# Kernel optimization log

Measured on AMD Instinct MI355X. Metric: run time of the kernel, lower is better.

Reference implementation:

```python
import jax, jax.numpy as jnp
import numpy as np

B = 8
C_IN = 3
DIV = 7
N0 = 20 * 4 ** DIV      # 327680 pixels at division 7
N1 = N0 // 4            # 81920 pixels at division 6
N2 = N1 // 4            # 20480 pixels at division 5
K_CONV = 10             # SpherePHD conv kernel size (triangle + 9 neighbors)
K_ADJ = 4               # pooling neighborhood (pixel + 3 edge-adjacent)


def setup_inputs() -> dict:
    key = jax.random.key(0)
    ks = jax.random.split(key, 15)
    x = jax.random.normal(ks[0], (B, C_IN, N0), dtype=jnp.float32)
    conv_t0 = jax.random.randint(ks[1], (N0, K_CONV), 0, N0, dtype=jnp.int32)
    conv_t1 = jax.random.randint(ks[2], (N1, K_CONV), 0, N1, dtype=jnp.int32)
    conv_t2 = jax.random.randint(ks[3], (N2, K_CONV), 0, N2, dtype=jnp.int32)
    adj0 = jax.random.randint(ks[4], (N0, K_ADJ), 0, N0, dtype=jnp.int32)
    adj1 = jax.random.randint(ks[5], (N1, K_ADJ), 0, N1, dtype=jnp.int32)
    pool0 = jax.random.randint(ks[6], (N1,), 0, N0, dtype=jnp.int32)
    pool1 = jax.random.randint(ks[7], (N2,), 0, N1, dtype=jnp.int32)
    w1 = jax.random.normal(ks[8], (16, C_IN, K_CONV), dtype=jnp.float32) * 0.1
    b1 = jax.random.normal(ks[9], (16,), dtype=jnp.float32) * 0.1
    w2 = jax.random.normal(ks[10], (32, 16, K_CONV), dtype=jnp.float32) * 0.1
    b2 = jax.random.normal(ks[11], (32,), dtype=jnp.float32) * 0.1
    w3 = jax.random.normal(ks[12], (10, 32, K_CONV), dtype=jnp.float32) * 0.1
    b3 = jax.random.normal(ks[13], (10,), dtype=jnp.float32) * 0.1
    return {"x": x, "conv_t0": conv_t0, "conv_t1": conv_t1, "conv_t2": conv_t2,
            "adj0": adj0, "adj1": adj1, "pool0": pool0, "pool1": pool1,
            "w1": w1, "b1": b1, "w2": w2, "b2": b2, "w3": w3, "b3": b3}


def phd_conv2d(x, table, w, b):
    # x: [B, Cin, N]; table: [N, K] neighbor indices; w: [Cout, Cin, K]
    g = x[:, :, table]                               # gather -> [B, Cin, N, K]
    return jnp.einsum('bcnk,ock->bon', g, w) + b[None, :, None]


def phd_maxpool(x, adj, pool):
    # max over adjacency neighborhood, then 4:1 downsample via pooling table
    m = jnp.max(x[:, :, adj], axis=-1)               # [B, C, N_fine]
    return m[:, :, pool]                             # [B, C, N_coarse]


def reference(x, conv_t0, conv_t1, conv_t2, adj0, adj1, pool0, pool1,
              w1, b1, w2, b2, w3, b3):
    h = phd_conv2d(x, conv_t0, w1, b1)               # [B, 16, N0]
    h = phd_maxpool(h, adj0, pool0)                  # [B, 16, N1]
    h = phd_conv2d(h, conv_t1, w2, b2)               # [B, 32, N1]
    h = phd_maxpool(h, adj1, pool1)                  # [B, 32, N2]
    h = phd_conv2d(h, conv_t2, w3, b3)               # [B, 10, N2]
    return jnp.mean(h, axis=-1)                      # PHD_avgpool -> [B, 10]
```

## Files before the change

### kernel.cpp

```cpp
#include <hip/hip_runtime.h>

#define NB 8
#define CIN 3
#define N0 327680
#define N1 81920
#define N2 20480
#define KC 10
#define KA 4

typedef __attribute__((ext_vector_type(8))) short bf16x8;
typedef __attribute__((ext_vector_type(4))) float f32x4;
typedef int4  __attribute__((aligned(4))) int4_u;

__device__ __forceinline__ unsigned f2bf(float f) {
  unsigned u = __float_as_uint(f);
  return (u + 0x7FFFu + ((u >> 16) & 1u)) >> 16;
}

union bfrag { bf16x8 v; unsigned u[4]; };

__global__ __launch_bounds__(256) void kpre(
    const float* __restrict__ x, uint4* __restrict__ xT64,
    const int* __restrict__ conv_t0, const int* __restrict__ conv_t1,
    const int* __restrict__ conv_t2,
    const int* __restrict__ adj0, const int* __restrict__ adj1,
    const int* __restrict__ pool0, const int* __restrict__ pool1,
    int* __restrict__ fidxM, int* __restrict__ fidxP, float* __restrict__ A12,
    const float* __restrict__ w1, const float* __restrict__ w2,
    const float* __restrict__ w3, const float* __restrict__ b3,
    unsigned short* __restrict__ wB1, unsigned short* __restrict__ wB,
    float* __restrict__ w3t, float* __restrict__ out) {
  int blk = blockIdx.x;
  if (blk < 1280) {
    int n = blk * 256 + threadIdx.x;
    unsigned d[12];
#pragma unroll
    for (int bp = 0; bp < 4; ++bp) {
      const float* pe = x + (size_t)(2 * bp) * CIN * N0 + n;
      const float* po = pe + (size_t)CIN * N0;
      float e0 = pe[0], e1 = pe[N0], e2 = pe[2 * N0];
      float o0 = po[0], o1 = po[N0], o2 = po[2 * N0];
      d[bp * 3 + 0] = f2bf(e0) | (f2bf(e1) << 16);
      d[bp * 3 + 1] = f2bf(e2) | (f2bf(o0) << 16);
      d[bp * 3 + 2] = f2bf(o1) | (f2bf(o2) << 16);
    }
    uint4* dst = xT64 + (size_t)n * 4;
    dst[0] = make_uint4(d[0], d[1], d[2], d[3]);
    dst[1] = make_uint4(d[4], d[5], d[6], d[7]);
    dst[2] = make_uint4(d[8], d[9], d[10], d[11]);
    dst[3] = make_uint4(0, 0, 0, 0);
  } else if (blk < 2560) {
    int t = (blk - 1280) * 256 + threadIdx.x;
    int j = t >> 2, p = t & 3;
    int pj = pool0[j];
    int pos = adj0[pj * KA + p];
    const int2* s0 = (const int2*)(conv_t0 + (size_t)pos * 10);
    int2 q0 = s0[0], q1 = s0[1], q2 = s0[2], q3 = s0[3], q4 = s0[4];
    int4_u* dM = (int4_u*)(fidxM + (size_t)t * 12);
    dM[0] = make_int4(q0.x * 64, q0.y * 64, q4.x * 64, q4.y * 64);
    dM[1] = make_int4(q1.x * 64, q1.y * 64, q2.x * 64, q2.y * 64);
    dM[2] = make_int4(q3.x * 64, q3.y * 64, 0, 0);
    if (j < N2) {
      int qj = pool1[j];
      int qos = adj1[qj * KA + p];
      const int2* s1 = (const int2*)(conv_t1 + (size_t)qos * 10);
      int2 r0 = s1[0], r1 = s1[1], r2 = s1[2], r3 = s1[3], r4 = s1[4];
      int4_u* dP = (int4_u*)(fidxP + (size_t)t * 12);
      dP[0] = make_int4(r0.x * 32, r1.x * 32, r2.x * 32, r3.x * 32);
      dP[1] = make_int4(r4.x * 32, 0,          r0.y * 32, r1.y * 32);
      dP[2] = make_int4(r2.y * 32, r3.y * 32, r4.y * 32, 0);
    }
  } else if (blk < 3360) {
    int t = (blk - 2560) * 256 + threadIdx.x;
    int n = conv_t2[t];
    int k = t % 10;
    atomicAdd(&A12[n * 12 + k], 1.0f);
  } else {
    int t = (blk - 3360) * 256 + threadIdx.x;
    if (t < 1024) {
      int ch = t >> 9, rest = t & 511, l = rest >> 3, e = rest & 7;
      int k = ch * 32 + ((l >> 4) * 8) + e;
      int tap = k >> 2, cc = k & 3;
      float v = (tap < KC && cc < CIN) ? w1[((l & 15) * CIN + cc) * KC + tap] : 0.f;
      wB1[t] = (unsigned short)f2bf(v);
    }
    if (t < 5120) {
      int e = t & 7, l = (t >> 3) & 63, nt = (t >> 9) & 1, q = t >> 10;
      int kc = q * 32 + ((l >> 4) * 8) + e;
      int tap = kc >> 4, c = kc & 15;
      int o = nt * 16 + (l & 15);
      wB[t] = (unsigned short)f2bf(w2[(o * 16 + c) * KC + tap]);
    }
    if (t < 3200) { int o = t % 10, r = t / 10, c = r & 31, k = r >> 5;
                    w3t[t] = w3[(o * 32 + c) * KC + k]; }
    if (t < 80)   out[t] = b3[t % 10];
  }
}

#define TR0(s) ((s) == 0 ? Ra.x : (s) == 1 ? Ra.w : (s) == 2 ? Rb.z : Rc.y)
#define TR1(s) ((s) == 0 ? Ra.y : (s) == 1 ? Rb.x : (s) == 2 ? Rb.w : Rc.z)
#define TR2(s) ((s) == 0 ? Ra.z : (s) == 1 ? Rb.y : (s) == 2 ? Rc.x : Rc.w)

__global__ __launch_bounds__(256, 4) void k1(
    const char* __restrict__ xT64, const int* __restrict__ fidxM,
    const bf16x8* __restrict__ wB1, const float* __restrict__ b1,
    unsigned short* __restrict__ h2) {
  int blk = blockIdx.x;
  int wave = threadIdx.x >> 6;
  int lane = threadIdx.x & 63;
  int col = lane & 15, hi = lane >> 4;
  int tile = blk * 4 + wave;
  bf16x8 B0 = wB1[lane];
  bf16x8 B1 = wB1[64 + lane];
  float bias = b1[col];
  int seloff = ((hi + 1) >> 1) << 2;

  int4 I = *(const int4_u*)(fidxM + ((size_t)tile * 16 + col) * 12 + seloff);
  int a0 = (hi == 2) ? I.z : I.x;
  int a1 = (hi == 2) ? I.w : I.y;
  const uint4* r0p = (const uint4*)(xT64 + a0);
  const uint4* r1p = (const uint4*)(xT64 + a1);
  uint4 R0a = r0p[0], R0b = r0p[1], R0c = r0p[2];
  uint4 R1a = r1p[0], R1b = r1p[1], R1c = r1p[2];
  uint4 zz = make_uint4(0, 0, 0, 0);
  uint4 R2a = zz, R2b = zz, R2c = zz, R3a = zz, R3b = zz, R3c = zz;
  if (hi == 0) {
    const uint4* r2p = (const uint4*)(xT64 + I.z);
    const uint4* r3p = (const uint4*)(xT64 + I.w);
    R2a = r2p[0]; R2b = r2p[1]; R2c = r2p[2];
    R3a = r3p[0]; R3b = r3p[1]; R3c = r3p[2];
  }
  size_t j = (size_t)tile * 4 + hi;
  unsigned short* dst = h2 + j * 16 + col;

#define DO_BPAIR(s)                                                           \
  {                                                                           \
    unsigned t0, t1, t2, u0, u1, u2, v0, v1, v2, w0, w1, w2;                  \
    { uint4 Ra = R0a, Rb = R0b, Rc = R0c;                                     \
      t0 = TR0(s); t1 = TR1(s); t2 = TR2(s); }                                \
    { uint4 Ra = R1a, Rb = R1b, Rc = R1c;                                     \
      u0 = TR0(s); u1 = TR1(s); u2 = TR2(s); }                                \
    { uint4 Ra = R2a, Rb = R2b, Rc = R2c;                                     \
      v0 = TR0(s); v1 = TR1(s); v2 = TR2(s); }                                \
    { uint4 Ra = R3a, Rb = R3b, Rc = R3c;                                     \
      w0 = TR0(s); w1 = TR1(s); w2 = TR2(s); }                                \
    bfrag A0c0, A1c0, A0c1, A1c1;                                             \
    A0c0.u[0] = t0; A0c0.u[1] = t1 & 0xFFFFu;                                 \
    A0c0.u[2] = u0; A0c0.u[3] = u1 & 0xFFFFu;                                 \
    A1c0.u[0] = (t1 >> 16) | (t2 << 16); A1c0.u[1] = t2 >> 16;                \
    A1c0.u[2] = (u1 >> 16) | (u2 << 16); A1c0.u[3] = u2 >> 16;                \
    A0c1.u[0] = v0; A0c1.u[1] = v1 & 0xFFFFu;                                 \
    A0c1.u[2] = w0; A0c1.u[3] = w1 & 0xFFFFu;                                 \
    A1c1.u[0] = (v1 >> 16) | (v2 << 16); A1c1.u[1] = v2 >> 16;                \
    A1c1.u[2] = (w1 >> 16) | (w2 << 16); A1c1.u[3] = w2 >> 16;                \
    f32x4 z = {0.f, 0.f, 0.f, 0.f};                                           \
    f32x4 acc0 = __builtin_amdgcn_mfma_f32_16x16x32_bf16(A0c0.v, B0, z, 0, 0, 0); \
    acc0 = __builtin_amdgcn_mfma_f32_16x16x32_bf16(A0c1.v, B1, acc0, 0, 0, 0);    \
    f32x4 acc1 = __builtin_amdgcn_mfma_f32_16x16x32_bf16(A1c0.v, B0, z, 0, 0, 0); \
    acc1 = __builtin_amdgcn_mfma_f32_16x16x32_bf16(A1c1.v, B1, acc1, 0, 0, 0);    \
    float m0 = fmaxf(fmaxf(acc0[0], acc0[1]), fmaxf(acc0[2], acc0[3])) + bias;    \
    float m1 = fmaxf(fmaxf(acc1[0], acc1[1]), fmaxf(acc1[2], acc1[3])) + bias;    \
    dst[(size_t)(2 * (s)) * N1 * 16]     = (unsigned short)f2bf(m0);          \
    dst[(size_t)(2 * (s) + 1) * N1 * 16] = (unsigned short)f2bf(m1);          \
  }
  DO_BPAIR(0)
  DO_BPAIR(1)
  DO_BPAIR(2)
  DO_BPAIR(3)
#undef DO_BPAIR
}

__global__ __launch_bounds__(256) void k2(
    const char* __restrict__ h2, const int* __restrict__ fidxP,
    const bf16x8* __restrict__ wB, const float* __restrict__ b2,
    float* __restrict__ h3) {
  int blk = blockIdx.x;
  int b = blk & 7;
  int wave = threadIdx.x >> 6;
  int lane = threadIdx.x & 63;
  int col = lane & 15;
  int odd = (lane >> 5) & 1;
  int tile0 = ((blk >> 3) * 4 + wave) * 8;
  const char* hb = h2 + (size_t)b * N1 * 32 + ((lane >> 4) & 1) * 16;

  bf16x8 Bf[10];
#pragma unroll
  for (int i = 0; i < 10; ++i) Bf[i] = wB[i * 64 + lane];
  float bias0 = b2[col];
  float bias1 = b2[16 + col];

#pragma unroll 2
  for (int i = 0; i < 8; ++i) {
    int tile = tile0 + i;
    const int* fp = fidxP + ((size_t)tile * 16 + col) * 12 + odd * 6;
    int4 T = *(const int4_u*)fp;
    int  T4 = fp[4];
    f32x4 acc0 = {0.f, 0.f, 0.f, 0.f};
    f32x4 acc1 = {0.f, 0.f, 0.f, 0.f};
    bf16x8 A;
    A = *(const bf16x8*)(hb + T.x);
    acc0 = __builtin_amdgcn_mfma_f32_16x16x32_bf16(A, Bf[0], acc0, 0, 0, 0);
    acc1 = __builtin_amdgcn_mfma_f32_16x16x32_bf16(A, Bf[1], acc1, 0, 0, 0);
    A = *(const bf16x8*)(hb + T.y);
    acc0 = __builtin_amdgcn_mfma_f32_16x16x32_bf16(A, Bf[2], acc0, 0, 0, 0);
    acc1 = __builtin_amdgcn_mfma_f32_16x16x32_bf16(A, Bf[3], acc1, 0, 0, 0);
    A = *(const bf16x8*)(hb + T.z);
    acc0 = __builtin_amdgcn_mfma_f32_16x16x32_bf16(A, Bf[4], acc0, 0, 0, 0);
    acc1 = __builtin_amdgcn_mfma_f32_16x16x32_bf16(A, Bf[5], acc1, 0, 0, 0);
    A = *(const bf16x8*)(hb + T.w);
    acc0 = __builtin_amdgcn_mfma_f32_16x16x32_bf16(A, Bf[6], acc0, 0, 0, 0);
    acc1 = __builtin_amdgcn_mfma_f32_16x16x32_bf16(A, Bf[7], acc1, 0, 0, 0);
    A = *(const bf16x8*)(hb + T4);
    acc0 = __builtin_amdgcn_mfma_f32_16x16x32_bf16(A, Bf[8], acc0, 0, 0, 0);
    acc1 = __builtin_amdgcn_mfma_f32_16x16x32_bf16(A, Bf[9], acc1, 0, 0, 0);
    float m0 = fmaxf(fmaxf(acc0[0], acc0[1]), fmaxf(acc0[2], acc0[3])) + bias0;
    float m1 = fmaxf(fmaxf(acc1[0], acc1[1]), fmaxf(acc1[2], acc1[3])) + bias1;
    int j = tile * 4 + (lane >> 4);
    float* dst = h3 + ((size_t)b * N2 + j) * 32 + col;
    dst[0]  = m0;
    dst[16] = m1;
  }
}

#define K3B_NCH 256
__global__ __launch_bounds__(256) void k3b(
    const float* __restrict__ h3, const float* __restrict__ A12,
    float* __restrict__ G) {
  __shared__ float SA[K3B_NCH * 12];
  __shared__ float GL[320];
  int blk = blockIdx.x;
  int b = blk & 7;
  int n0 = (blk >> 3) * K3B_NCH;
  int tid = threadIdx.x;
  const float4* src = (const float4*)(A12 + (size_t)n0 * 12);
#pragma unroll
  for (int i = 0; i < 3; ++i)
    ((float4*)SA)[tid + i * 256] = src[tid + i * 256];
  for (int i = tid; i < 320; i += 256) GL[i] = 0.f;
  __syncthreads();
  int wave = tid >> 6, lane = tid & 63;
  int c = lane & 31, nh = lane >> 5;
  float acc[10];
#pragma unroll
  for (int o = 0; o < 10; ++o) acc[o] = 0.f;
#pragma unroll 4
  for (int s = 0; s < K3B_NCH / 8; ++s) {
    int nl = s * 8 + wave * 2 + nh;
    float hv = h3[((size_t)b * N2 + n0 + nl) * 32 + c];
    const float4* ar = (const float4*)(SA + nl * 12);
    float4 a0 = ar[0], a1 = ar[1], a2 = ar[2];
    acc[0] += hv * a0.x; acc[1] += hv * a0.y;
    acc[2] += hv * a0.z; acc[3] += hv * a0.w;
    acc[4] += hv * a1.x; acc[5] += hv * a1.y;
    acc[6] += hv * a1.z; acc[7] += hv * a1.w;
    acc[8] += hv * a2.x; acc[9] += hv * a2.y;
  }
#pragma unroll
  for (int o = 0; o < 10; ++o) acc[o] += __shfl_xor(acc[o], 32);
  if (lane < 32) {
#pragma unroll
    for (int o = 0; o < 10; ++o) atomicAdd(&GL[c * 10 + o], acc[o]);
  }
  __syncthreads();
  for (int i = tid; i < 320; i += 256)
    atomicAdd(&G[b * 320 + i], GL[i]);
}

__global__ __launch_bounds__(256) void k3c(
    const float* __restrict__ G, const float* __restrict__ w3t,
    float* __restrict__ out) {
  int t = blockIdx.x * 256 + threadIdx.x;
  int pair = t >> 5, c = t & 31;
  int b = pair / 10, o = pair % 10;
  float s = 0.f;
#pragma unroll
  for (int k = 0; k < KC; ++k)
    s += G[b * 320 + c * 10 + k] * w3t[k * 320 + c * 10 + o];
#pragma unroll
  for (int off = 1; off < 32; off <<= 1) s += __shfl_xor(s, off);
  if ((threadIdx.x & 31) == 0) atomicAdd(&out[pair], s * (1.0f / N2));
}

extern "C" void kernel_launch(void* const* d_in, const int* in_sizes, int n_in,
                              void* d_out, int out_size, void* d_ws, size_t ws_size,
                              hipStream_t stream) {
  const float* x       = (const float*)d_in[0];
  const int*   conv_t0 = (const int*)d_in[1];
  const int*   conv_t1 = (const int*)d_in[2];
  const int*   conv_t2 = (const int*)d_in[3];
  const int*   adj0    = (const int*)d_in[4];
  const int*   adj1    = (const int*)d_in[5];
  const int*   pool0   = (const int*)d_in[6];
  const int*   pool1   = (const int*)d_in[7];
  const float* w1      = (const float*)d_in[8];
  const float* b1      = (const float*)d_in[9];
  const float* w2      = (const float*)d_in[10];
  const float* b2      = (const float*)d_in[11];
  const float* w3      = (const float*)d_in[12];
  const float* b3      = (const float*)d_in[13];
  float* out  = (float*)d_out;
  float* wsf  = (float*)d_ws;

  float* h3b   = wsf;
  uint4* xT64  = (uint4*)wsf;
  unsigned short* h2b = (unsigned short*)(wsf + 5242880);
  int* fidxM   = (int*)(wsf + 2 * 5242880);
  int* fidxP   = fidxM + (size_t)N1 * 4 * 12;
  float* A12   = (float*)(fidxP + (size_t)N2 * 4 * 12);
  float* G     = A12 + (size_t)N2 * 12;
  unsigned short* wB1 = (unsigned short*)(G + 2560);
  unsigned short* wB  = wB1 + 1024;
  float* w3t   = (float*)(wB + 5120);

  hipMemsetAsync(A12, 0, (size_t)(N2 * 12 + 2560) * 4, stream);
  kpre<<<3380, 256, 0, stream>>>(x, xT64, conv_t0, conv_t1, conv_t2,
                                 adj0, adj1, pool0, pool1,
                                 fidxM, fidxP, A12,
                                 w1, w2, w3, b3, wB1, wB, w3t, out);
  k1<<<5120, 256, 0, stream>>>((const char*)xT64, fidxM, (const bf16x8*)wB1, b1, h2b);
  k2<<<1280, 256, 0, stream>>>((const char*)h2b, fidxP, (const bf16x8*)wB, b2, h3b);
  k3b<<<8 * (N2 / K3B_NCH), 256, 0, stream>>>(h3b, A12, G);
  k3c<<<10, 256, 0, stream>>>(G, w3t, out);
}
```

Baseline: 140.5 us.

## Fuse final conv reduction into k2 epilogue, eliminate h3 buffer and k3b

The k2 epilogue now multiplies each pooled conv2 output directly by the per-pixel A12 coefficients and accumulates per-channel partial sums in registers. These are reduced with cross-lane shuffles and shared-memory atomics, then added into G with global atomics. This removes the h3 intermediate write and re-read and the separate k3b launch. In exchange it adds 20 accumulator registers per thread under a 4-waves occupancy bound, plus per-block atomics in k2.

```diff
diff --git a/kernel.cpp b/kernel.cpp
--- a/kernel.cpp
+++ b/kernel.cpp
@@ -170,10 +170,11 @@
 #undef DO_BPAIR
 }
 
-__global__ __launch_bounds__(256) void k2(
+__global__ __launch_bounds__(256, 4) void k2(
     const char* __restrict__ h2, const int* __restrict__ fidxP,
-    const bf16x8* __restrict__ wB, const float* __restrict__ b2,
-    float* __restrict__ h3) {
+    const float* __restrict__ A12, const bf16x8* __restrict__ wB,
+    const float* __restrict__ b2, float* __restrict__ G) {
+  __shared__ float GL[320];
   int blk = blockIdx.x;
   int b = blk & 7;
   int wave = threadIdx.x >> 6;
@@ -182,12 +183,17 @@
   int odd = (lane >> 5) & 1;
   int tile0 = ((blk >> 3) * 4 + wave) * 8;
   const char* hb = h2 + (size_t)b * N1 * 32 + ((lane >> 4) & 1) * 16;
+  for (int i = threadIdx.x; i < 320; i += 256) GL[i] = 0.f;
+  __syncthreads();
 
   bf16x8 Bf[10];
 #pragma unroll
   for (int i = 0; i < 10; ++i) Bf[i] = wB[i * 64 + lane];
   float bias0 = b2[col];
   float bias1 = b2[16 + col];
+  float g0[10], g1[10];
+#pragma unroll
+  for (int k = 0; k < 10; ++k) { g0[k] = 0.f; g1[k] = 0.f; }
 
 #pragma unroll 2
   for (int i = 0; i < 8; ++i) {
@@ -216,53 +222,31 @@
     float m0 = fmaxf(fmaxf(acc0[0], acc0[1]), fmaxf(acc0[2], acc0[3])) + bias0;
     float m1 = fmaxf(fmaxf(acc1[0], acc1[1]), fmaxf(acc1[2], acc1[3])) + bias1;
     int j = tile * 4 + (lane >> 4);
-    float* dst = h3 + ((size_t)b * N2 + j) * 32 + col;
-    dst[0]  = m0;
-    dst[16] = m1;
-  }
-}
-
-#define K3B_NCH 256
-__global__ __launch_bounds__(256) void k3b(
-    const float* __restrict__ h3, const float* __restrict__ A12,
-    float* __restrict__ G) {
-  __shared__ float SA[K3B_NCH * 12];
-  __shared__ float GL[320];
-  int blk = blockIdx.x;
-  int b = blk & 7;
-  int n0 = (blk >> 3) * K3B_NCH;
-  int tid = threadIdx.x;
-  const float4* src = (const float4*)(A12 + (size_t)n0 * 12);
-#pragma unroll
-  for (int i = 0; i < 3; ++i)
-    ((float4*)SA)[tid + i * 256] = src[tid + i * 256];
-  for (int i = tid; i < 320; i += 256) GL[i] = 0.f;
+    const float* ar = A12 + (size_t)j * 12;
+    float4 a0 = *(const float4*)ar;
+    float4 a1 = *(const float4*)(ar + 4);
+    float2 a2 = *(const float2*)(ar + 8);
+    float av[10] = {a0.x, a0.y, a0.z, a0.w, a1.x, a1.y, a1.z, a1.w, a2.x, a2.y};
+#pragma unroll
+    for (int k = 0; k < 10; ++k) {
+      g0[k] = fmaf(m0, av[k], g0[k]);
+      g1[k] = fmaf(m1, av[k], g1[k]);
+    }
+  }
+#pragma unroll
+  for (int k = 0; k < 10; ++k) {
+    g0[k] += __shfl_xor(g0[k], 16); g0[k] += __shfl_xor(g0[k], 32);
+    g1[k] += __shfl_xor(g1[k], 16); g1[k] += __shfl_xor(g1[k], 32);
+  }
+  if (lane < 16) {
+#pragma unroll
+    for (int k = 0; k < 10; ++k) {
+      atomicAdd(&GL[col * 10 + k], g0[k]);
+      atomicAdd(&GL[(col + 16) * 10 + k], g1[k]);
+    }
+  }
   __syncthreads();
-  int wave = tid >> 6, lane = tid & 63;
-  int c = lane & 31, nh = lane >> 5;
-  float acc[10];
-#pragma unroll
-  for (int o = 0; o < 10; ++o) acc[o] = 0.f;
-#pragma unroll 4
-  for (int s = 0; s < K3B_NCH / 8; ++s) {
-    int nl = s * 8 + wave * 2 + nh;
-    float hv = h3[((size_t)b * N2 + n0 + nl) * 32 + c];
-    const float4* ar = (const float4*)(SA + nl * 12);
-    float4 a0 = ar[0], a1 = ar[1], a2 = ar[2];
-    acc[0] += hv * a0.x; acc[1] += hv * a0.y;
-    acc[2] += hv * a0.z; acc[3] += hv * a0.w;
-    acc[4] += hv * a1.x; acc[5] += hv * a1.y;
-    acc[6] += hv * a1.z; acc[7] += hv * a1.w;
-    acc[8] += hv * a2.x; acc[9] += hv * a2.y;
-  }
-#pragma unroll
-  for (int o = 0; o < 10; ++o) acc[o] += __shfl_xor(acc[o], 32);
-  if (lane < 32) {
-#pragma unroll
-    for (int o = 0; o < 10; ++o) atomicAdd(&GL[c * 10 + o], acc[o]);
-  }
-  __syncthreads();
-  for (int i = tid; i < 320; i += 256)
+  for (int i = threadIdx.x; i < 320; i += 256)
     atomicAdd(&G[b * 320 + i], GL[i]);
 }
 
@@ -301,7 +285,6 @@
   float* out  = (float*)d_out;
   float* wsf  = (float*)d_ws;
 
-  float* h3b   = wsf;
   uint4* xT64  = (uint4*)wsf;
   unsigned short* h2b = (unsigned short*)(wsf + 5242880);
   int* fidxM   = (int*)(wsf + 2 * 5242880);
@@ -318,7 +301,6 @@
                                  fidxM, fidxP, A12,
                                  w1, w2, w3, b3, wB1, wB, w3t, out);
   k1<<<5120, 256, 0, stream>>>((const char*)xT64, fidxM, (const bf16x8*)wB1, b1, h2b);
-  k2<<<1280, 256, 0, stream>>>((const char*)h2b, fidxP, (const bf16x8*)wB, b2, h3b);
-  k3b<<<8 * (N2 / K3B_NCH), 256, 0, stream>>>(h3b, A12, G);
+  k2<<<1280, 256, 0, stream>>>((const char*)h2b, fidxP, A12, (const bf16x8*)wB, b2, G);
   k3c<<<10, 256, 0, stream>>>(G, w3t, out);
 }
```

After: 131.9 us (median of 2 runs). 6.1% less time.
